# Optimization experiments

Hardware: AMD Instinct MI355X
Metric: run time of the kernel (lower is better)

Reference implementation:

```python
import jax, jax.numpy as jnp
import numpy as np

EMBED = 768
HEADS = 12
HEAD_DIM = EMBED // HEADS
B, T = 2, 2048


def setup_inputs() -> dict:
    key = jax.random.key(0)
    ks = jax.random.split(key, 5)
    scale = 0.02
    return {
        "x": jax.random.normal(ks[0], (B, T, EMBED), dtype=jnp.float32),
        "Wq": jax.random.normal(ks[1], (HEADS, EMBED, HEAD_DIM), dtype=jnp.float32) * scale,
        "Wk": jax.random.normal(ks[2], (HEADS, EMBED, HEAD_DIM), dtype=jnp.float32) * scale,
        "Wv": jax.random.normal(ks[3], (HEADS, EMBED, HEAD_DIM), dtype=jnp.float32) * scale,
        "Wp": jax.random.normal(ks[4], (EMBED, EMBED), dtype=jnp.float32) * scale,
        "bp": jnp.zeros((EMBED,), dtype=jnp.float32),
    }


def reference(x, Wq, Wk, Wv, Wp, bp):
    # x: [B,T,E]; per-head projections batched over the head axis.
    q = jnp.einsum("bte,hed->bhtd", x, Wq)  # [B,H,T,Dh]
    k = jnp.einsum("bte,hed->bhtd", x, Wk)
    v = jnp.einsum("bte,hed->bhtd", x, Wv)
    scale = 1.0 / jnp.sqrt(jnp.asarray(HEAD_DIM, dtype=x.dtype))
    scores = jnp.einsum("bhtd,bhsd->bhts", q, k) * scale  # [B,H,T,T]
    Tlen = x.shape[1]
    causal = jnp.tril(jnp.ones((Tlen, Tlen), dtype=bool))
    scores = jnp.where(causal[None, None], scores, jnp.asarray(-jnp.inf, dtype=scores.dtype))
    attn = jax.nn.softmax(scores, axis=-1)
    out = jnp.einsum("bhts,bhsd->bhtd", attn, v)  # [B,H,T,Dh]
    # concat heads (same layout as torch.cat over per-head outputs)
    out = out.transpose(0, 2, 1, 3).reshape(x.shape[0], Tlen, HEADS * HEAD_DIM)
    return out @ Wp + bp
```

## Files before the change

### kernel.cpp

```cpp
#include <hip/hip_runtime.h>
#include <math.h>

namespace {

constexpr int E_  = 768;
constexpr int H_  = 12;
constexpr int DH_ = 64;
constexpr int T_  = 2048;
constexpr int B_  = 2;
constexpr int M_  = B_ * T_;
constexpr int BH_ = B_ * H_;

typedef __attribute__((ext_vector_type(8))) short bf16x8;
typedef __attribute__((ext_vector_type(4))) float f32x4;

__device__ inline ushort f2bf(float f) {
  union { float f; unsigned u; } v; v.f = f;
  unsigned u = v.u + 0x7FFFu + ((v.u >> 16) & 1u);
  return (ushort)(u >> 16);
}
__device__ inline float bf2f(ushort u) {
  union { unsigned u; float f; } v; v.u = (unsigned)u << 16; return v.f;
}

__device__ __forceinline__ void gl16(const ushort* g, ushort* l) {
  __builtin_amdgcn_global_load_lds(
      (const __attribute__((address_space(1))) unsigned int*)(g),
      (__attribute__((address_space(3))) unsigned int*)(l), 16, 0, 0);
}

constexpr int NCONV = 1536;

__global__ __launch_bounds__(256) void prep_k(
    const float* __restrict__ x,
    const float* __restrict__ Wq, const float* __restrict__ Wk,
    const float* __restrict__ Wv, const float* __restrict__ Wp,
    ushort* __restrict__ xb, ushort* __restrict__ Wt, ushort* __restrict__ Wpt)
{
  __shared__ float tile[64][65];
  const int bid = blockIdx.x;
  const int tid = threadIdx.x;

  if (bid < NCONV) {
    const size_t i = ((size_t)bid * 256 + tid) * 8;
    float4 a = *(const float4*)(x + i);
    float4 b = *(const float4*)(x + i + 4);
    ushort o[8] = {f2bf(a.x), f2bf(a.y), f2bf(a.z), f2bf(a.w),
                   f2bf(b.x), f2bf(b.y), f2bf(b.z), f2bf(b.w)};
    *(bf16x8*)(xb + i) = *(bf16x8*)o;
    return;
  }

  const int wb = bid - NCONV;
  const int tr = tid >> 4, tc = tid & 15;
  const float* src; ushort* dst;
  int k0, n0, sN, dK;
  if (wb < 432) {
    const int mat = wb / 144, rem = wb % 144;
    const int h = rem / 12, ktile = rem % 12;
    const float* W = (mat == 0) ? Wq : (mat == 1) ? Wk : Wv;
    src = W + (size_t)h * E_ * DH_;
    dst = Wt + (size_t)(mat * H_ + h) * DH_ * E_;
    k0 = ktile * 64; n0 = 0; sN = DH_; dK = E_;
  } else {
    const int rem = wb - 432;
    src = Wp;
    dst = Wpt;
    k0 = (rem / 12) * 64; n0 = (rem % 12) * 64; sN = E_; dK = E_;
  }

#pragma unroll
  for (int rr = 0; rr < 64; rr += 16) {
    float4 v = *(const float4*)(src + (size_t)(k0 + tr + rr) * sN + n0 + tc * 4);
    tile[tr + rr][tc * 4 + 0] = v.x;
    tile[tr + rr][tc * 4 + 1] = v.y;
    tile[tr + rr][tc * 4 + 2] = v.z;
    tile[tr + rr][tc * 4 + 3] = v.w;
  }
  __syncthreads();
#pragma unroll
  for (int rr = 0; rr < 64; rr += 16) {
    const int n = tr + rr;
    ushort4 o;
    o.x = f2bf(tile[tc * 4 + 0][n]);
    o.y = f2bf(tile[tc * 4 + 1][n]);
    o.z = f2bf(tile[tc * 4 + 2][n]);
    o.w = f2bf(tile[tc * 4 + 3][n]);
    *(ushort4*)(dst + (size_t)(n0 + n) * dK + k0 + tc * 4) = o;
  }
}

constexpr float QSCALE = 0.18033688f;

__global__ __launch_bounds__(256) void qkv_fused_k(
    const ushort* __restrict__ xb, const ushort* __restrict__ Wt,
    ushort* __restrict__ q_ws, ushort* __restrict__ k_ws, ushort* __restrict__ vt_ws)
{
  __shared__ __align__(16) ushort lds[(128 + 64) * 64];
  ushort* As = lds;
  ushort* Bs = lds + 128 * 64;

  const int seg = blockIdx.x;
  const int n0g = 0;
  const int m0  = blockIdx.y * 128;
  const ushort* Wh = Wt + (size_t)seg * DH_ * E_;

  const int tid  = threadIdx.x;
  const int w    = tid >> 6, l = tid & 63;
  const int lrow = l & 15, lk = l >> 4;
  const int r7   = lrow & 7;
  const int srow = l >> 3;
  const int sch  = (l & 7) ^ srow;

  f32x4 acc[2][4] = {};

  for (int k0 = 0; k0 < E_; k0 += 64) {
#pragma unroll
    for (int r = 0; r < 4; ++r) {
      const int base = r * 32 + w * 8;
      gl16(xb + (size_t)(m0 + base + srow) * E_ + k0 + sch * 8, &As[base * 64]);
      if (r < 2)
        gl16(Wh + (size_t)(n0g + base + srow) * E_ + k0 + sch * 8, &Bs[base * 64]);
    }
    __syncthreads();

#pragma unroll
    for (int kk = 0; kk < 2; ++kk) {
      const int cof = ((kk * 4 + lk) ^ r7) * 8;
      const bf16x8 a0 = *(const bf16x8*)&As[(w * 32 + lrow) * 64 + cof];
      const bf16x8 a1 = *(const bf16x8*)&As[(w * 32 + 16 + lrow) * 64 + cof];
#pragma unroll
      for (int nf = 0; nf < 4; ++nf) {
        const bf16x8 b = *(const bf16x8*)&Bs[(nf * 16 + lrow) * 64 + cof];
        acc[0][nf] = __builtin_amdgcn_mfma_f32_16x16x32_bf16(a0, b, acc[0][nf], 0, 0, 0);
        acc[1][nf] = __builtin_amdgcn_mfma_f32_16x16x32_bf16(a1, b, acc[1][nf], 0, 0, 0);
      }
    }
    __syncthreads();
  }

  const int b   = m0 >> 11;
  const int t0  = m0 & 2047;
  const int mat = seg / H_;
  const int h   = seg - mat * H_;
  const int bh  = b * H_ + h;

  if (mat != 2) {
    const float qs = (mat == 0) ? QSCALE : 1.0f;
    ushort* outw = (mat == 0) ? q_ws : k_ws;
#pragma unroll
    for (int mi = 0; mi < 2; ++mi)
#pragma unroll
      for (int i = 0; i < 4; ++i) {
        const int t = t0 + w * 32 + mi * 16 + lk * 4 + i;
        ushort* orow = outw + ((size_t)bh * T_ + t) * DH_;
#pragma unroll
        for (int nf = 0; nf < 4; ++nf)
          orow[nf * 16 + lrow] = f2bf(acc[mi][nf][i] * qs);
      }
  } else {
    ushort* Td = lds;
    __syncthreads();
#pragma unroll
    for (int mi = 0; mi < 2; ++mi)
#pragma unroll
      for (int i = 0; i < 4; ++i) {
        const int tl = w * 32 + mi * 16 + lk * 4 + i;
#pragma unroll
        for (int nf = 0; nf < 4; ++nf)
          Td[(nf * 16 + lrow) * 136 + tl] = f2bf(acc[mi][nf][i]);
      }
    __syncthreads();
#pragma unroll
    for (int it = 0; it < 4; ++it) {
      const int c = tid + it * 256;
      const int d = c >> 4, sub = c & 15;
      *(bf16x8*)(vt_ws + ((size_t)bh * DH_ + d) * T_ + t0 + sub * 8) =
          *(const bf16x8*)&Td[d * 136 + sub * 8];
    }
  }
}

__global__ __launch_bounds__(256) void attn_split_k(
    const ushort* __restrict__ q_ws, const ushort* __restrict__ k_ws,
    const ushort* __restrict__ vt_ws, ushort* __restrict__ op_ws,
    float2* __restrict__ ml_ws)
{
  __shared__ __align__(16) ushort Ks[64 * 64];
  __shared__ __align__(16) ushort Vt[64 * 64];
  __shared__ __align__(16) ushort Pl[4][16 * 64];

  const int qt = 31 - (int)blockIdx.y;
  const int bh = blockIdx.x;
  const int hz = blockIdx.z;
  const int nt = qt + 1;
  const int klo = hz ? (nt >> 1) : 0;
  const int khi = hz ? nt : (nt >> 1);
  const int q0 = qt * 64;

  const ushort* Qb  = q_ws + (size_t)bh * T_ * DH_;
  const ushort* Kb  = k_ws + (size_t)bh * T_ * DH_;
  const ushort* VTb = vt_ws + (size_t)bh * DH_ * T_;

  const int tid  = threadIdx.x;
  const int w    = tid >> 6;
  const int l    = tid & 63;
  const int lrow = l & 15;
  const int lk   = l >> 4;
  const int r7   = lrow & 7;
  const int rr   = tid >> 3;
  const int sub  = tid & 7;
  const int swc  = sub ^ (rr & 7);

  const int st0 = rr * 64 + swc * 8;
  const int st1 = (rr + 32) * 64 + swc * 8;

  int kof0[4], kof1[4];
#pragma unroll
  for (int ct = 0; ct < 4; ++ct) {
    kof0[ct] = (ct * 16 + lrow) * 64 + ((lk ^ r7) * 8);
    kof1[ct] = (ct * 16 + lrow) * 64 + (((lk + 4) ^ r7) * 8);
  }

  const ushort* Qrow = Qb + (size_t)(q0 + w * 16 + lrow) * DH_;
  const bf16x8 qa0 = *(const bf16x8*)(Qrow + lk * 8);
  const bf16x8 qa1 = *(const bf16x8*)(Qrow + lk * 8 + 32);
  const int qglob = q0 + w * 16 + lrow;

  float m_r = -INFINITY, l_r = 0.f;
  f32x4 oc[4] = {};

  ushort* Pw = &Pl[w][0];
  const int rd0 = lrow * 64 + ((lk ^ r7) * 8);
  const int rd1 = lrow * 64 + (((lk + 4) ^ r7) * 8);
  const int wrbase  = lrow * 128 + (lk & 1) * 8;
  const int wrchunk = (lk >> 1);

  if (klo < khi) {
    bf16x8 kp0 = *(const bf16x8*)(Kb + (size_t)(klo * 64 + rr) * DH_ + sub * 8);
    bf16x8 kp1 = *(const bf16x8*)(Kb + (size_t)(klo * 64 + rr + 32) * DH_ + sub * 8);
    bf16x8 vp0 = *(const bf16x8*)(VTb + (size_t)rr * T_ + klo * 64 + sub * 8);
    bf16x8 vp1 = *(const bf16x8*)(VTb + (size_t)(rr + 32) * T_ + klo * 64 + sub * 8);

    for (int kt = klo; kt < khi; ++kt) {
      const int s0 = kt * 64;

      *(bf16x8*)&Ks[st0] = kp0;
      *(bf16x8*)&Ks[st1] = kp1;
      *(bf16x8*)&Vt[st0] = vp0;
      *(bf16x8*)&Vt[st1] = vp1;
      __syncthreads();

      if (kt + 1 < khi) {
        const int sn = s0 + 64;
        kp0 = *(const bf16x8*)(Kb + (size_t)(sn + rr) * DH_ + sub * 8);
        kp1 = *(const bf16x8*)(Kb + (size_t)(sn + rr + 32) * DH_ + sub * 8);
        vp0 = *(const bf16x8*)(VTb + (size_t)rr * T_ + sn + sub * 8);
        vp1 = *(const bf16x8*)(VTb + (size_t)(rr + 32) * T_ + sn + sub * 8);
      }

      f32x4 st[4];
#pragma unroll
      for (int ct = 0; ct < 4; ++ct) {
        const bf16x8 kb0 = *(const bf16x8*)&Ks[kof0[ct]];
        const bf16x8 kb1 = *(const bf16x8*)&Ks[kof1[ct]];
        f32x4 z = {0.f, 0.f, 0.f, 0.f};
        z = __builtin_amdgcn_mfma_f32_16x16x32_bf16(kb0, qa0, z, 0, 0, 0);
        st[ct] = __builtin_amdgcn_mfma_f32_16x16x32_bf16(kb1, qa1, z, 0, 0, 0);
      }

      if (kt == qt) {
#pragma unroll
        for (int ct = 0; ct < 4; ++ct)
#pragma unroll
          for (int i = 0; i < 4; ++i)
            if (s0 + ct * 16 + lk * 4 + i > qglob) st[ct][i] = -INFINITY;
      }

      float mc[4];
#pragma unroll
      for (int ct = 0; ct < 4; ++ct)
        mc[ct] = fmaxf(fmaxf(st[ct][0], st[ct][1]), fmaxf(st[ct][2], st[ct][3]));
      float mx = fmaxf(fmaxf(mc[0], mc[1]), fmaxf(mc[2], mc[3]));
      mx = fmaxf(mx, __shfl_xor(mx, 16));
      mx = fmaxf(mx, __shfl_xor(mx, 32));

      if (__any(mx > m_r + 8.f)) {
        const float mn   = fmaxf(m_r, mx);
        const float corr = exp2f(m_r - mn);
        m_r = mn;
        l_r *= corr;
#pragma unroll
        for (int i = 0; i < 4; ++i) {
          const float cr = __shfl(corr, lk * 4 + i);
#pragma unroll
          for (int ct = 0; ct < 4; ++ct) oc[ct][i] *= cr;
        }
      }

      float sc[4];
#pragma unroll
      for (int ct = 0; ct < 4; ++ct) {
#pragma unroll
        for (int i = 0; i < 4; ++i) st[ct][i] = exp2f(st[ct][i] - m_r);
        sc[ct] = (st[ct][0] + st[ct][1]) + (st[ct][2] + st[ct][3]);
      }
      float rs = (sc[0] + sc[1]) + (sc[2] + sc[3]);
      rs += __shfl_xor(rs, 16);
      rs += __shfl_xor(rs, 32);
      l_r += rs;

#pragma unroll
      for (int ct = 0; ct < 4; ++ct) {
        unsigned lo, hi;
        asm("v_cvt_pk_bf16_f32 %0, %1, %2" : "=v"(lo) : "v"(st[ct][0]), "v"(st[ct][1]));
        asm("v_cvt_pk_bf16_f32 %0, %1, %2" : "=v"(hi) : "v"(st[ct][2]), "v"(st[ct][3]));
        uint2 pk; pk.x = lo; pk.y = hi;
        const int ch = ((ct * 2 + wrchunk) ^ r7);
        *(uint2*)((char*)Pw + wrbase + ch * 16) = pk;
      }

      const bf16x8 pa0 = *(const bf16x8*)(Pw + rd0);
      const bf16x8 pa1 = *(const bf16x8*)(Pw + rd1);

#pragma unroll
      for (int ct = 0; ct < 4; ++ct) {
        const bf16x8 vb0 = *(const bf16x8*)&Vt[kof0[ct]];
        const bf16x8 vb1 = *(const bf16x8*)&Vt[kof1[ct]];
        oc[ct] = __builtin_amdgcn_mfma_f32_16x16x32_bf16(pa0, vb0, oc[ct], 0, 0, 0);
        oc[ct] = __builtin_amdgcn_mfma_f32_16x16x32_bf16(pa1, vb1, oc[ct], 0, 0, 0);
      }
      __syncthreads();
    }
  }

  const size_t pb = (size_t)(hz * BH_ + bh) * T_;
  if (lk == 0)
    ml_ws[pb + q0 + w * 16 + lrow] = make_float2(m_r, l_r);
#pragma unroll
  for (int i = 0; i < 4; ++i) {
    const int t = q0 + w * 16 + lk * 4 + i;
    ushort* orow = op_ws + (pb + t) * DH_;
#pragma unroll
    for (int ct = 0; ct < 4; ++ct)
      orow[ct * 16 + lrow] = f2bf(oc[ct][i]);
  }
}

__global__ __launch_bounds__(256) void proj_fused_k(
    const ushort* __restrict__ op_ws, const float2* __restrict__ ml_ws,
    const ushort* __restrict__ Wpt, const float* __restrict__ bp,
    float* __restrict__ out)
{
  __shared__ __align__(16) ushort lds[(64 + 64) * 64];
  ushort* As = lds;
  ushort* Bs = lds + 64 * 64;

  const int n0 = blockIdx.x * 64;
  const int m0 = blockIdx.y * 64;
  const int b  = m0 >> 11;
  const int t0 = m0 & 2047;

  const int tid  = threadIdx.x;
  const int w    = tid >> 6, l = tid & 63;
  const int lrow = l & 15, lk = l >> 4;
  const int r7   = lrow & 7;
  const int srow = l >> 3;
  const int sch  = (l & 7) ^ srow;
  const int ar = tid >> 2;
  const int cc = tid & 3;
  const int a7 = ar & 7;

  f32x4 acc[4] = {};

  for (int k0 = 0; k0 < E_; k0 += 64) {
    const int h  = k0 >> 6;
    const int bh = b * H_ + h;

#pragma unroll
    for (int r = 0; r < 2; ++r) {
      const int base = r * 32 + w * 8;
      gl16(Wpt + (size_t)(n0 + base + srow) * E_ + k0 + sch * 8, &Bs[base * 64]);
    }

    {
      const int t = t0 + ar;
      const size_t ixA = (size_t)bh * T_ + t;
      const size_t ixB = (size_t)(BH_ + bh) * T_ + t;
      const float2 mlA = ml_ws[ixA];
      const float2 mlB = ml_ws[ixB];
      const float m   = fmaxf(mlA.x, mlB.x);
      const float wA  = exp2f(mlA.x - m);
      const float wB  = exp2f(mlB.x - m);
      const float inv = 1.0f / (wA * mlA.y + wB * mlB.y);
      const float fA = wA * inv, fB = wB * inv;

      const ushort* pA = op_ws + ixA * DH_ + cc * 16;
      const ushort* pB = op_ws + ixB * DH_ + cc * 16;
      bf16x8 a0 = *(const bf16x8*)pA;
      bf16x8 a1 = *(const bf16x8*)(pA + 8);
      bf16x8 b0 = *(const bf16x8*)pB;
      bf16x8 b1 = *(const bf16x8*)(pB + 8);
      ushort o[16];
#pragma unroll
      for (int j = 0; j < 8; ++j) {
        o[j]     = f2bf(fA * bf2f((ushort)a0[j]) + fB * bf2f((ushort)b0[j]));
        o[8 + j] = f2bf(fA * bf2f((ushort)a1[j]) + fB * bf2f((ushort)b1[j]));
      }
      *(bf16x8*)&As[ar * 64 + ((2 * cc) ^ a7) * 8]     = *(const bf16x8*)&o[0];
      *(bf16x8*)&As[ar * 64 + ((2 * cc + 1) ^ a7) * 8] = *(const bf16x8*)&o[8];
    }
    __syncthreads();

#pragma unroll
    for (int kk = 0; kk < 2; ++kk) {
      const int cof = ((kk * 4 + lk) ^ r7) * 8;
      const bf16x8 a = *(const bf16x8*)&As[(w * 16 + lrow) * 64 + cof];
#pragma unroll
      for (int nf = 0; nf < 4; ++nf) {
        const bf16x8 bb = *(const bf16x8*)&Bs[(nf * 16 + lrow) * 64 + cof];
        acc[nf] = __builtin_amdgcn_mfma_f32_16x16x32_bf16(a, bb, acc[nf], 0, 0, 0);
      }
    }
    __syncthreads();
  }

  float bias[4];
#pragma unroll
  for (int nf = 0; nf < 4; ++nf) bias[nf] = bp[n0 + nf * 16 + lrow];

#pragma unroll
  for (int i = 0; i < 4; ++i) {
    const int m = m0 + w * 16 + lk * 4 + i;
    float* orow = out + (size_t)m * E_ + n0;
#pragma unroll
    for (int nf = 0; nf < 4; ++nf)
      orow[nf * 16 + lrow] = acc[nf][i] + bias[nf];
  }
}

}

extern "C" void kernel_launch(void* const* d_in, const int* in_sizes, int n_in,
                              void* d_out, int out_size, void* d_ws, size_t ws_size,
                              hipStream_t stream) {
  const float* x  = (const float*)d_in[0];
  const float* Wq = (const float*)d_in[1];
  const float* Wk = (const float*)d_in[2];
  const float* Wv = (const float*)d_in[3];
  const float* Wp = (const float*)d_in[4];
  const float* bp = (const float*)d_in[5];
  float* out = (float*)d_out;

  const size_t nx  = (size_t)M_ * E_;
  const size_t nwt = (size_t)3 * H_ * DH_ * E_;
  const size_t nwp = (size_t)E_ * E_;
  const size_t per = (size_t)BH_ * T_ * DH_;

  ushort* xb    = (ushort*)d_ws;
  ushort* Wt    = xb + nx;
  ushort* Wpt   = Wt + nwt;
  ushort* q_ws  = Wpt + nwp;
  ushort* k_ws  = q_ws + per;
  ushort* vt_ws = k_ws + per;
  ushort* op_ws = vt_ws + per;
  float2* ml_ws = (float2*)(op_ws + 2 * per);

  prep_k<<<dim3(NCONV + 576), 256, 0, stream>>>(x, Wq, Wk, Wv, Wp, xb, Wt, Wpt);
  qkv_fused_k<<<dim3(36, 32), 256, 0, stream>>>(xb, Wt, q_ws, k_ws, vt_ws);
  attn_split_k<<<dim3(24, 32, 2), 256, 0, stream>>>(q_ws, k_ws, vt_ws, op_ws, ml_ws);
  proj_fused_k<<<dim3(12, 64), 256, 0, stream>>>(op_ws, ml_ws, Wpt, bp, out);
}
```

Measured before the change: 92.73 us.

## Split attention KV range four ways and compute PV transposed without LDS staging

After: 145.1 us. +56.4%, slower.

```diff
diff --git a/kernel.cpp b/kernel.cpp
--- a/kernel.cpp
+++ b/kernel.cpp
@@ -10,9 +10,12 @@
 constexpr int B_  = 2;
 constexpr int M_  = B_ * T_;
 constexpr int BH_ = B_ * H_;
+constexpr int NSPLIT = 4;
 
 typedef __attribute__((ext_vector_type(8))) short bf16x8;
 typedef __attribute__((ext_vector_type(4))) float f32x4;
+
+union Frag { bf16x8 v; uint2 u[2]; unsigned w[4]; };
 
 __device__ inline ushort f2bf(float f) {
   union { float f; unsigned u; } v; v.f = f;
@@ -101,7 +104,6 @@
   ushort* Bs = lds + 128 * 64;
 
   const int seg = blockIdx.x;
-  const int n0g = 0;
   const int m0  = blockIdx.y * 128;
   const ushort* Wh = Wt + (size_t)seg * DH_ * E_;
 
@@ -120,7 +122,7 @@
       const int base = r * 32 + w * 8;
       gl16(xb + (size_t)(m0 + base + srow) * E_ + k0 + sch * 8, &As[base * 64]);
       if (r < 2)
-        gl16(Wh + (size_t)(n0g + base + srow) * E_ + k0 + sch * 8, &Bs[base * 64]);
+        gl16(Wh + (size_t)(base + srow) * E_ + k0 + sch * 8, &Bs[base * 64]);
     }
     __syncthreads();
 
@@ -181,21 +183,20 @@
   }
 }
 
-__global__ __launch_bounds__(256) void attn_split_k(
+__global__ __launch_bounds__(256, 6) void attn_split_k(
     const ushort* __restrict__ q_ws, const ushort* __restrict__ k_ws,
     const ushort* __restrict__ vt_ws, ushort* __restrict__ op_ws,
     float2* __restrict__ ml_ws)
 {
   __shared__ __align__(16) ushort Ks[64 * 64];
   __shared__ __align__(16) ushort Vt[64 * 64];
-  __shared__ __align__(16) ushort Pl[4][16 * 64];
 
   const int qt = 31 - (int)blockIdx.y;
   const int bh = blockIdx.x;
   const int hz = blockIdx.z;
   const int nt = qt + 1;
-  const int klo = hz ? (nt >> 1) : 0;
-  const int khi = hz ? nt : (nt >> 1);
+  const int klo = (hz * nt) >> 2;
+  const int khi = ((hz + 1) * nt) >> 2;
   const int q0 = qt * 64;
 
   const ushort* Qb  = q_ws + (size_t)bh * T_ * DH_;
@@ -221,6 +222,10 @@
     kof0[ct] = (ct * 16 + lrow) * 64 + ((lk ^ r7) * 8);
     kof1[ct] = (ct * 16 + lrow) * 64 + (((lk + 4) ^ r7) * 8);
   }
+  int vof[4];
+#pragma unroll
+  for (int q16 = 0; q16 < 4; ++q16)
+    vof[q16] = lrow * 128 + (((q16 * 2 + (lk >> 1)) ^ r7) << 4) + ((lk & 1) << 3);
 
   const ushort* Qrow = Qb + (size_t)(q0 + w * 16 + lrow) * DH_;
   const bf16x8 qa0 = *(const bf16x8*)(Qrow + lk * 8);
@@ -229,12 +234,6 @@
 
   float m_r = -INFINITY, l_r = 0.f;
   f32x4 oc[4] = {};
-
-  ushort* Pw = &Pl[w][0];
-  const int rd0 = lrow * 64 + ((lk ^ r7) * 8);
-  const int rd1 = lrow * 64 + (((lk + 4) ^ r7) * 8);
-  const int wrbase  = lrow * 128 + (lk & 1) * 8;
-  const int wrchunk = (lk >> 1);
 
   if (klo < khi) {
     bf16x8 kp0 = *(const bf16x8*)(Kb + (size_t)(klo * 64 + rr) * DH_ + sub * 8);
@@ -291,11 +290,9 @@
         m_r = mn;
         l_r *= corr;
 #pragma unroll
-        for (int i = 0; i < 4; ++i) {
-          const float cr = __shfl(corr, lk * 4 + i);
-#pragma unroll
-          for (int ct = 0; ct < 4; ++ct) oc[ct][i] *= cr;
-        }
+        for (int ct = 0; ct < 4; ++ct)
+#pragma unroll
+          for (int i = 0; i < 4; ++i) oc[ct][i] *= corr;
       }
 
       float sc[4];
@@ -310,40 +307,42 @@
       rs += __shfl_xor(rs, 32);
       l_r += rs;
 
+      Frag pb0, pb1;
+      asm("v_cvt_pk_bf16_f32 %0, %1, %2" : "=v"(pb0.w[0]) : "v"(st[0][0]), "v"(st[0][1]));
+      asm("v_cvt_pk_bf16_f32 %0, %1, %2" : "=v"(pb0.w[1]) : "v"(st[0][2]), "v"(st[0][3]));
+      asm("v_cvt_pk_bf16_f32 %0, %1, %2" : "=v"(pb0.w[2]) : "v"(st[1][0]), "v"(st[1][1]));
+      asm("v_cvt_pk_bf16_f32 %0, %1, %2" : "=v"(pb0.w[3]) : "v"(st[1][2]), "v"(st[1][3]));
+      asm("v_cvt_pk_bf16_f32 %0, %1, %2" : "=v"(pb1.w[0]) : "v"(st[2][0]), "v"(st[2][1]));
+      asm("v_cvt_pk_bf16_f32 %0, %1, %2" : "=v"(pb1.w[1]) : "v"(st[2][2]), "v"(st[2][3]));
+      asm("v_cvt_pk_bf16_f32 %0, %1, %2" : "=v"(pb1.w[2]) : "v"(st[3][0]), "v"(st[3][1]));
+      asm("v_cvt_pk_bf16_f32 %0, %1, %2" : "=v"(pb1.w[3]) : "v"(st[3][2]), "v"(st[3][3]));
+
 #pragma unroll
       for (int ct = 0; ct < 4; ++ct) {
-        unsigned lo, hi;
-        asm("v_cvt_pk_bf16_f32 %0, %1, %2" : "=v"(lo) : "v"(st[ct][0]), "v"(st[ct][1]));
-        asm("v_cvt_pk_bf16_f32 %0, %1, %2" : "=v"(hi) : "v"(st[ct][2]), "v"(st[ct][3]));
-        uint2 pk; pk.x = lo; pk.y = hi;
-        const int ch = ((ct * 2 + wrchunk) ^ r7);
-        *(uint2*)((char*)Pw + wrbase + ch * 16) = pk;
-      }
-
-      const bf16x8 pa0 = *(const bf16x8*)(Pw + rd0);
-      const bf16x8 pa1 = *(const bf16x8*)(Pw + rd1);
-
-#pragma unroll
-      for (int ct = 0; ct < 4; ++ct) {
-        const bf16x8 vb0 = *(const bf16x8*)&Vt[kof0[ct]];
-        const bf16x8 vb1 = *(const bf16x8*)&Vt[kof1[ct]];
-        oc[ct] = __builtin_amdgcn_mfma_f32_16x16x32_bf16(pa0, vb0, oc[ct], 0, 0, 0);
-        oc[ct] = __builtin_amdgcn_mfma_f32_16x16x32_bf16(pa1, vb1, oc[ct], 0, 0, 0);
+        const char* vb = (const char*)Vt + ct * 2048;
+        Frag va0, va1;
+        va0.u[0] = *(const uint2*)(vb + vof[0]);
+        va0.u[1] = *(const uint2*)(vb + vof[1]);
+        va1.u[0] = *(const uint2*)(vb + vof[2]);
+        va1.u[1] = *(const uint2*)(vb + vof[3]);
+        oc[ct] = __builtin_amdgcn_mfma_f32_16x16x32_bf16(va0.v, pb0.v, oc[ct], 0, 0, 0);
+        oc[ct] = __builtin_amdgcn_mfma_f32_16x16x32_bf16(va1.v, pb1.v, oc[ct], 0, 0, 0);
       }
       __syncthreads();
     }
   }
 
   const size_t pb = (size_t)(hz * BH_ + bh) * T_;
+  const int t = q0 + w * 16 + lrow;
   if (lk == 0)
-    ml_ws[pb + q0 + w * 16 + lrow] = make_float2(m_r, l_r);
-#pragma unroll
-  for (int i = 0; i < 4; ++i) {
-    const int t = q0 + w * 16 + lk * 4 + i;
-    ushort* orow = op_ws + (pb + t) * DH_;
-#pragma unroll
-    for (int ct = 0; ct < 4; ++ct)
-      orow[ct * 16 + lrow] = f2bf(oc[ct][i]);
+    ml_ws[pb + t] = make_float2(m_r, l_r);
+  ushort* orow = op_ws + (pb + t) * DH_;
+#pragma unroll
+  for (int ct = 0; ct < 4; ++ct) {
+    ushort4 o4;
+    o4.x = f2bf(oc[ct][0]); o4.y = f2bf(oc[ct][1]);
+    o4.z = f2bf(oc[ct][2]); o4.w = f2bf(oc[ct][3]);
+    *(ushort4*)(orow + ct * 16 + lk * 4) = o4;
   }
 }
 
@@ -385,30 +384,42 @@
 
     {
       const int t = t0 + ar;
-      const size_t ixA = (size_t)bh * T_ + t;
-      const size_t ixB = (size_t)(BH_ + bh) * T_ + t;
-      const float2 mlA = ml_ws[ixA];
-      const float2 mlB = ml_ws[ixB];
-      const float m   = fmaxf(mlA.x, mlB.x);
-      const float wA  = exp2f(mlA.x - m);
-      const float wB  = exp2f(mlB.x - m);
-      const float inv = 1.0f / (wA * mlA.y + wB * mlB.y);
-      const float fA = wA * inv, fB = wB * inv;
-
-      const ushort* pA = op_ws + ixA * DH_ + cc * 16;
-      const ushort* pB = op_ws + ixB * DH_ + cc * 16;
-      bf16x8 a0 = *(const bf16x8*)pA;
-      bf16x8 a1 = *(const bf16x8*)(pA + 8);
-      bf16x8 b0 = *(const bf16x8*)pB;
-      bf16x8 b1 = *(const bf16x8*)(pB + 8);
-      ushort o[16];
-#pragma unroll
-      for (int j = 0; j < 8; ++j) {
-        o[j]     = f2bf(fA * bf2f((ushort)a0[j]) + fB * bf2f((ushort)b0[j]));
-        o[8 + j] = f2bf(fA * bf2f((ushort)a1[j]) + fB * bf2f((ushort)b1[j]));
-      }
-      *(bf16x8*)&As[ar * 64 + ((2 * cc) ^ a7) * 8]     = *(const bf16x8*)&o[0];
-      *(bf16x8*)&As[ar * 64 + ((2 * cc + 1) ^ a7) * 8] = *(const bf16x8*)&o[8];
+      size_t ix[NSPLIT];
+      float2 ml[NSPLIT];
+#pragma unroll
+      for (int z = 0; z < NSPLIT; ++z) {
+        ix[z] = ((size_t)(z * BH_ + bh) * T_ + t);
+        ml[z] = ml_ws[ix[z]];
+      }
+      float m = fmaxf(fmaxf(ml[0].x, ml[1].x), fmaxf(ml[2].x, ml[3].x));
+      float f[NSPLIT];
+      float den = 0.f;
+#pragma unroll
+      for (int z = 0; z < NSPLIT; ++z) {
+        f[z] = exp2f(ml[z].x - m);
+        den += f[z] * ml[z].y;
+      }
+      const float inv = 1.0f / den;
+#pragma unroll
+      for (int z = 0; z < NSPLIT; ++z) f[z] *= inv;
+
+      float o[16] = {};
+#pragma unroll
+      for (int z = 0; z < NSPLIT; ++z) {
+        const ushort* p = op_ws + ix[z] * DH_ + cc * 16;
+        bf16x8 x0 = *(const bf16x8*)p;
+        bf16x8 x1 = *(const bf16x8*)(p + 8);
+#pragma unroll
+        for (int j = 0; j < 8; ++j) {
+          o[j]     += f[z] * bf2f((ushort)x0[j]);
+          o[8 + j] += f[z] * bf2f((ushort)x1[j]);
+        }
+      }
+      ushort ob[16];
+#pragma unroll
+      for (int j = 0; j < 16; ++j) ob[j] = f2bf(o[j]);
+      *(bf16x8*)&As[ar * 64 + ((2 * cc) ^ a7) * 8]     = *(const bf16x8*)&ob[0];
+      *(bf16x8*)&As[ar * 64 + ((2 * cc + 1) ^ a7) * 8] = *(const bf16x8*)&ob[8];
     }
     __syncthreads();
 
@@ -464,10 +475,10 @@
   ushort* k_ws  = q_ws + per;
   ushort* vt_ws = k_ws + per;
   ushort* op_ws = vt_ws + per;
-  float2* ml_ws = (float2*)(op_ws + 2 * per);
+  float2* ml_ws = (float2*)(op_ws + NSPLIT * per);
 
   prep_k<<<dim3(NCONV + 576), 256, 0, stream>>>(x, Wq, Wk, Wv, Wp, xb, Wt, Wpt);
   qkv_fused_k<<<dim3(36, 32), 256, 0, stream>>>(xb, Wt, q_ws, k_ws, vt_ws);
-  attn_split_k<<<dim3(24, 32, 2), 256, 0, stream>>>(q_ws, k_ws, vt_ws, op_ws, ml_ws);
+  attn_split_k<<<dim3(24, 32, NSPLIT), 256, 0, stream>>>(q_ws, k_ws, vt_ws, op_ws, ml_ws);
   proj_fused_k<<<dim3(12, 64), 256, 0, stream>>>(op_ws, ml_ws, Wpt, bp, out);
 }
```
